# Performance work log

Measured on AMD Instinct MI355X. Metric: run time of the kernel, lower is better.

The kernel has to match this reference:

```python
import jax, jax.numpy as jnp
import numpy as np

OUT_H, OUT_W = 7, 7          # aligned_height, aligned_width
SPATIAL_SCALE = 0.25         # stride-4 feature level
SAMPLE_NUM = 2               # 2x2 bilinear samples per bin


def setup_inputs() -> dict:
    key = jax.random.key(0)
    kf, kb, kx, ky, kw, kh = jax.random.split(key, 6)
    B, C, H, W = 4, 256, 200, 272
    features = jax.random.normal(kf, (B, C, H, W), dtype=jnp.float32)
    N = 1024
    img_w = W / SPATIAL_SCALE  # boxes live in image coords
    img_h = H / SPATIAL_SCALE
    bi = jax.random.randint(kb, (N,), 0, B).astype(jnp.float32)
    x1 = jax.random.uniform(kx, (N,), dtype=jnp.float32) * (img_w - 260.0)
    y1 = jax.random.uniform(ky, (N,), dtype=jnp.float32) * (img_h - 260.0)
    bw = 16.0 + jax.random.uniform(kw, (N,), dtype=jnp.float32) * 240.0
    bh = 16.0 + jax.random.uniform(kh, (N,), dtype=jnp.float32) * 240.0
    rois = jnp.stack([bi, x1, y1, x1 + bw, y1 + bh], axis=1)  # [N,5]
    return {"features": features, "rois": rois}


def _roi_align(features, rois):
    B, C, H, W = features.shape
    N = rois.shape[0]
    sn = SAMPLE_NUM
    feats = jnp.transpose(features, (0, 2, 3, 1))  # [B,H,W,C] channel-last for gathers

    b = rois[:, 0].astype(jnp.int32)
    x1 = rois[:, 1] * SPATIAL_SCALE
    y1 = rois[:, 2] * SPATIAL_SCALE
    x2 = rois[:, 3] * SPATIAL_SCALE
    y2 = rois[:, 4] * SPATIAL_SCALE
    roi_w = jnp.maximum(x2 - x1, 1.0)
    roi_h = jnp.maximum(y2 - y1, 1.0)
    bin_w = roi_w / OUT_W
    bin_h = roi_h / OUT_H

    # flattened sample positions: y = y1 + (p + 0.5)/sn * bin_h,  p in [0, OUT_H*sn)
    py = (jnp.arange(OUT_H * sn, dtype=jnp.float32) + 0.5) / sn
    px = (jnp.arange(OUT_W * sn, dtype=jnp.float32) + 0.5) / sn
    ys = y1[:, None] + py[None, :] * bin_h[:, None]  # [N, Hs]
    xs = x1[:, None] + px[None, :] * bin_w[:, None]  # [N, Ws]

    valid = ((ys > -1.0) & (ys < H))[:, :, None] & ((xs > -1.0) & (xs < W))[:, None, :]

    y = jnp.clip(ys, 0.0, H - 1.0)
    x = jnp.clip(xs, 0.0, W - 1.0)
    y0 = jnp.clip(jnp.floor(y), 0.0, H - 2.0)
    x0 = jnp.clip(jnp.floor(x), 0.0, W - 2.0)
    ly = y - y0
    lx = x - x0
    hy = 1.0 - ly
    hx = 1.0 - lx
    y0i = y0.astype(jnp.int32)
    x0i = x0.astype(jnp.int32)
    y1i = y0i + 1
    x1i = x0i + 1

    bN = b[:, None, None]

    def g(yi, xi):  # gather corner values -> [N, Hs, Ws, C]
        return feats[bN, yi[:, :, None], xi[:, None, :]]

    w00 = (hy[:, :, None] * hx[:, None, :])[..., None]
    w01 = (hy[:, :, None] * lx[:, None, :])[..., None]
    w10 = (ly[:, :, None] * hx[:, None, :])[..., None]
    w11 = (ly[:, :, None] * lx[:, None, :])[..., None]

    val = (w00 * g(y0i, x0i) + w01 * g(y0i, x1i)
           + w10 * g(y1i, x0i) + w11 * g(y1i, x1i))
    val = jnp.where(valid[..., None], val, 0.0)

    # average the sn x sn samples per bin
    val = val.reshape(N, OUT_H, sn, OUT_W, sn, C).mean(axis=(2, 4))  # [N,OUT_H,OUT_W,C]
    return jnp.transpose(val, (0, 3, 1, 2))  # [N, C, OUT_H, OUT_W]


def reference(features, rois):
    return _roi_align(features, rois)
```

## Files before the change

### kernel.cpp

```cpp
#include <hip/hip_runtime.h>
#include <hip/hip_bf16.h>

#define B_ 4
#define C_ 256
#define H_ 200
#define W_ 272
#define OH 7
#define OW 7

__global__ void detect_dtype(const float* __restrict__ rois_f, int* __restrict__ flag) {
  if (threadIdx.x == 0 && blockIdx.x == 0) {
    bool ok = true;
    for (int k = 0; k < 8; ++k) {
      float v = rois_f[5 * k];
      ok = ok && (v >= 0.0f) && (v < 4.0f) && (v == floorf(v)) && (v == v);
    }
    *flag = ok ? 0 : 1;
  }
}

template <typename T> __device__ __forceinline__ float to_f(T v);
template <> __device__ __forceinline__ float to_f<float>(float v) { return v; }
template <> __device__ __forceinline__ float to_f<__hip_bfloat16>(__hip_bfloat16 v) {
  return __bfloat162float(v);
}
template <typename T> __device__ __forceinline__ T from_f(float v);
template <> __device__ __forceinline__ float from_f<float>(float v) { return v; }
template <> __device__ __forceinline__ __hip_bfloat16 from_f<__hip_bfloat16>(float v) {
  return __float2bfloat16(v);
}

template <typename T>
__device__ __forceinline__ void roi_align_body(const T* __restrict__ feats,
                                               const T* __restrict__ rois,
                                               T* __restrict__ out, int idx) {
  int pw = idx % OW;
  int ph = (idx / OW) % OH;
  int c  = (idx / (OW * OH)) % C_;
  int n  = idx / (OW * OH * C_);

  const T* r = rois + (size_t)n * 5;
  int   b  = (int)to_f<T>(r[0]);
  float x1 = to_f<T>(r[1]) * 0.25f;
  float y1 = to_f<T>(r[2]) * 0.25f;
  float x2 = to_f<T>(r[3]) * 0.25f;
  float y2 = to_f<T>(r[4]) * 0.25f;

  float bin_w = fmaxf(x2 - x1, 1.0f) * (1.0f / 7.0f);
  float bin_h = fmaxf(y2 - y1, 1.0f) * (1.0f / 7.0f);

  const T* fp = feats + ((size_t)b * C_ + c) * (size_t)(H_ * W_);

  float sum = 0.0f;
#pragma unroll
  for (int iy = 0; iy < 2; ++iy) {
    float ys = y1 + ((float)(ph * 2 + iy) + 0.5f) * 0.5f * bin_h;
    bool vy = (ys > -1.0f) && (ys < (float)H_);
    float y  = fminf(fmaxf(ys, 0.0f), (float)(H_ - 1));
    float y0f = fminf(floorf(y), (float)(H_ - 2));
    float ly = y - y0f;
    float hy = 1.0f - ly;
    int y0 = (int)y0f;

#pragma unroll
    for (int ix = 0; ix < 2; ++ix) {
      float xs = x1 + ((float)(pw * 2 + ix) + 0.5f) * 0.5f * bin_w;
      bool vx = (xs > -1.0f) && (xs < (float)W_);
      float x  = fminf(fmaxf(xs, 0.0f), (float)(W_ - 1));
      float x0f = fminf(floorf(x), (float)(W_ - 2));
      float lx = x - x0f;
      float hx = 1.0f - lx;
      int x0 = (int)x0f;

      const T* p = fp + y0 * W_ + x0;
      float v00 = to_f<T>(p[0]);
      float v01 = to_f<T>(p[1]);
      float v10 = to_f<T>(p[W_]);
      float v11 = to_f<T>(p[W_ + 1]);
      float v = hy * (hx * v00 + lx * v01) + ly * (hx * v10 + lx * v11);
      if (vy && vx) sum += v;
    }
  }

  out[idx] = from_f<T>(sum * 0.25f);
}

__global__ __launch_bounds__(256) void roi_align_kernel(
    const void* __restrict__ feats, const void* __restrict__ rois,
    void* __restrict__ out, const int* __restrict__ flag, int total) {
  int idx = blockIdx.x * blockDim.x + threadIdx.x;
  if (idx >= total) return;
  if (*flag == 0) {
    roi_align_body<float>((const float*)feats, (const float*)rois, (float*)out, idx);
  } else {
    roi_align_body<__hip_bfloat16>((const __hip_bfloat16*)feats,
                                   (const __hip_bfloat16*)rois,
                                   (__hip_bfloat16*)out, idx);
  }
}

extern "C" void kernel_launch(void* const* d_in, const int* in_sizes, int n_in,
                              void* d_out, int out_size, void* d_ws, size_t ws_size,
                              hipStream_t stream) {
  const void* feats = d_in[0];
  const void* rois  = d_in[1];
  int* flag = (int*)d_ws;

  detect_dtype<<<1, 64, 0, stream>>>((const float*)rois, flag);

  int total = out_size;
  int threads = 256;
  int blocks = (total + threads - 1) / threads;
  roi_align_kernel<<<blocks, threads, 0, stream>>>(feats, rois, d_out, flag, total);
}
```

Before: 460.2 us.

## Transpose features to NHWC in workspace and gather per-ROI across channels

Adds a tiled shared-memory NCHW-to-NHWC transpose into the workspace, then a per-ROI kernel where each thread handles one channel, so the bilinear corner loads are contiguous across a wavefront. Results are staged in shared memory and written back in the NCHW output order. It also removes the runtime dtype-detection launch and the bf16 path. This trades an extra full pass over the ~223MB feature tensor (read plus write) for coalesced gathers, and depends on the workspace being large enough, otherwise it falls back to the direct kernel.

```diff
diff --git a/kernel.cpp b/kernel.cpp
--- a/kernel.cpp
+++ b/kernel.cpp
@@ -1,56 +1,118 @@
 #include <hip/hip_runtime.h>
-#include <hip/hip_bf16.h>
 
 #define B_ 4
 #define C_ 256
 #define H_ 200
 #define W_ 272
+#define HW_ (H_ * W_)
 #define OH 7
 #define OW 7
+#define NROI 1024
 
-__global__ void detect_dtype(const float* __restrict__ rois_f, int* __restrict__ flag) {
-  if (threadIdx.x == 0 && blockIdx.x == 0) {
-    bool ok = true;
-    for (int k = 0; k < 8; ++k) {
-      float v = rois_f[5 * k];
-      ok = ok && (v >= 0.0f) && (v < 4.0f) && (v == floorf(v)) && (v == v);
-    }
-    *flag = ok ? 0 : 1;
+__global__ __launch_bounds__(256) void nchw_to_nhwc(
+    const float* __restrict__ in, float* __restrict__ out) {
+  __shared__ float tile[32][33];
+  int hw0 = blockIdx.x * 32;
+  int c0  = blockIdx.y * 32;
+  int b   = blockIdx.z;
+  int t = threadIdx.x;
+
+  int lhw = t & 31, lc = t >> 5;
+#pragma unroll
+  for (int i = 0; i < 4; ++i) {
+    int c = c0 + lc + i * 8;
+    tile[lc + i * 8][lhw] = in[((size_t)b * C_ + c) * HW_ + hw0 + lhw];
+  }
+  __syncthreads();
+  int wc = t & 31, whw = t >> 5;
+#pragma unroll
+  for (int i = 0; i < 4; ++i) {
+    int hw = hw0 + whw + i * 8;
+    out[((size_t)b * HW_ + hw) * C_ + c0 + wc] = tile[wc][whw + i * 8];
   }
 }
 
-template <typename T> __device__ __forceinline__ float to_f(T v);
-template <> __device__ __forceinline__ float to_f<float>(float v) { return v; }
-template <> __device__ __forceinline__ float to_f<__hip_bfloat16>(__hip_bfloat16 v) {
-  return __bfloat162float(v);
-}
-template <typename T> __device__ __forceinline__ T from_f(float v);
-template <> __device__ __forceinline__ float from_f<float>(float v) { return v; }
-template <> __device__ __forceinline__ __hip_bfloat16 from_f<__hip_bfloat16>(float v) {
-  return __float2bfloat16(v);
+__global__ __launch_bounds__(256) void roi_gather_nhwc(
+    const float* __restrict__ nhwc, const float* __restrict__ rois,
+    float* __restrict__ out) {
+  __shared__ float acc[C_ * 51];
+  int n = blockIdx.x;
+  int c = threadIdx.x;
+
+  const float* r = rois + (size_t)n * 5;
+  int   b  = (int)r[0];
+  float x1 = r[1] * 0.25f;
+  float y1 = r[2] * 0.25f;
+  float x2 = r[3] * 0.25f;
+  float y2 = r[4] * 0.25f;
+  float bin_w = fmaxf(x2 - x1, 1.0f) * (1.0f / 7.0f);
+  float bin_h = fmaxf(y2 - y1, 1.0f) * (1.0f / 7.0f);
+
+  const float* fb = nhwc + (size_t)b * HW_ * C_ + c;
+
+  for (int s = 0; s < 49; ++s) {
+    int ph = s / 7, pw = s % 7;
+    float sum = 0.0f;
+#pragma unroll
+    for (int iy = 0; iy < 2; ++iy) {
+      float ys = y1 + ((float)(ph * 2 + iy) + 0.5f) * 0.5f * bin_h;
+      bool vy = (ys > -1.0f) && (ys < (float)H_);
+      float y  = fminf(fmaxf(ys, 0.0f), (float)(H_ - 1));
+      float y0f = fminf(floorf(y), (float)(H_ - 2));
+      float ly = y - y0f;
+      float hy = 1.0f - ly;
+      int y0 = (int)y0f;
+#pragma unroll
+      for (int ix = 0; ix < 2; ++ix) {
+        float xs = x1 + ((float)(pw * 2 + ix) + 0.5f) * 0.5f * bin_w;
+        bool vx = (xs > -1.0f) && (xs < (float)W_);
+        float x  = fminf(fmaxf(xs, 0.0f), (float)(W_ - 1));
+        float x0f = fminf(floorf(x), (float)(W_ - 2));
+        float lx = x - x0f;
+        float hx = 1.0f - lx;
+        int x0 = (int)x0f;
+
+        const float* p = fb + (size_t)(y0 * W_ + x0) * C_;
+        float v00 = p[0];
+        float v01 = p[C_];
+        float v10 = p[W_ * C_];
+        float v11 = p[W_ * C_ + C_];
+        float v = hy * (hx * v00 + lx * v01) + ly * (hx * v10 + lx * v11);
+        if (vy && vx) sum += v;
+      }
+    }
+    acc[c * 51 + s] = sum * 0.25f;
+  }
+  __syncthreads();
+
+  float* o = out + (size_t)n * (C_ * 49);
+  for (int j = c; j < C_ * 49; j += 256) {
+    int cc = j / 49;
+    int ss = j - cc * 49;
+    o[j] = acc[cc * 51 + ss];
+  }
 }
 
-template <typename T>
-__device__ __forceinline__ void roi_align_body(const T* __restrict__ feats,
-                                               const T* __restrict__ rois,
-                                               T* __restrict__ out, int idx) {
+__global__ __launch_bounds__(256) void roi_align_direct(
+    const float* __restrict__ feats, const float* __restrict__ rois,
+    float* __restrict__ out, int total) {
+  int idx = blockIdx.x * blockDim.x + threadIdx.x;
+  if (idx >= total) return;
   int pw = idx % OW;
   int ph = (idx / OW) % OH;
   int c  = (idx / (OW * OH)) % C_;
   int n  = idx / (OW * OH * C_);
 
-  const T* r = rois + (size_t)n * 5;
-  int   b  = (int)to_f<T>(r[0]);
-  float x1 = to_f<T>(r[1]) * 0.25f;
-  float y1 = to_f<T>(r[2]) * 0.25f;
-  float x2 = to_f<T>(r[3]) * 0.25f;
-  float y2 = to_f<T>(r[4]) * 0.25f;
-
+  const float* r = rois + (size_t)n * 5;
+  int   b  = (int)r[0];
+  float x1 = r[1] * 0.25f;
+  float y1 = r[2] * 0.25f;
+  float x2 = r[3] * 0.25f;
+  float y2 = r[4] * 0.25f;
   float bin_w = fmaxf(x2 - x1, 1.0f) * (1.0f / 7.0f);
   float bin_h = fmaxf(y2 - y1, 1.0f) * (1.0f / 7.0f);
 
-  const T* fp = feats + ((size_t)b * C_ + c) * (size_t)(H_ * W_);
-
+  const float* fp = feats + ((size_t)b * C_ + c) * (size_t)HW_;
   float sum = 0.0f;
 #pragma unroll
   for (int iy = 0; iy < 2; ++iy) {
@@ -58,58 +120,40 @@
     bool vy = (ys > -1.0f) && (ys < (float)H_);
     float y  = fminf(fmaxf(ys, 0.0f), (float)(H_ - 1));
     float y0f = fminf(floorf(y), (float)(H_ - 2));
-    float ly = y - y0f;
-    float hy = 1.0f - ly;
+    float ly = y - y0f, hy = 1.0f - ly;
     int y0 = (int)y0f;
-
 #pragma unroll
     for (int ix = 0; ix < 2; ++ix) {
       float xs = x1 + ((float)(pw * 2 + ix) + 0.5f) * 0.5f * bin_w;
       bool vx = (xs > -1.0f) && (xs < (float)W_);
       float x  = fminf(fmaxf(xs, 0.0f), (float)(W_ - 1));
       float x0f = fminf(floorf(x), (float)(W_ - 2));
-      float lx = x - x0f;
-      float hx = 1.0f - lx;
+      float lx = x - x0f, hx = 1.0f - lx;
       int x0 = (int)x0f;
-
-      const T* p = fp + y0 * W_ + x0;
-      float v00 = to_f<T>(p[0]);
-      float v01 = to_f<T>(p[1]);
-      float v10 = to_f<T>(p[W_]);
-      float v11 = to_f<T>(p[W_ + 1]);
-      float v = hy * (hx * v00 + lx * v01) + ly * (hx * v10 + lx * v11);
+      const float* p = fp + y0 * W_ + x0;
+      float v = hy * (hx * p[0] + lx * p[1]) + ly * (hx * p[W_] + lx * p[W_ + 1]);
       if (vy && vx) sum += v;
     }
   }
-
-  out[idx] = from_f<T>(sum * 0.25f);
-}
-
-__global__ __launch_bounds__(256) void roi_align_kernel(
-    const void* __restrict__ feats, const void* __restrict__ rois,
-    void* __restrict__ out, const int* __restrict__ flag, int total) {
-  int idx = blockIdx.x * blockDim.x + threadIdx.x;
-  if (idx >= total) return;
-  if (*flag == 0) {
-    roi_align_body<float>((const float*)feats, (const float*)rois, (float*)out, idx);
-  } else {
-    roi_align_body<__hip_bfloat16>((const __hip_bfloat16*)feats,
-                                   (const __hip_bfloat16*)rois,
-                                   (__hip_bfloat16*)out, idx);
-  }
+  out[idx] = sum * 0.25f;
 }
 
 extern "C" void kernel_launch(void* const* d_in, const int* in_sizes, int n_in,
                               void* d_out, int out_size, void* d_ws, size_t ws_size,
                               hipStream_t stream) {
-  const void* feats = d_in[0];
-  const void* rois  = d_in[1];
-  int* flag = (int*)d_ws;
+  const float* feats = (const float*)d_in[0];
+  const float* rois  = (const float*)d_in[1];
+  float* out = (float*)d_out;
 
-  detect_dtype<<<1, 64, 0, stream>>>((const float*)rois, flag);
+  const size_t nhwc_bytes = (size_t)B_ * HW_ * C_ * sizeof(float);
 
-  int total = out_size;
-  int threads = 256;
-  int blocks = (total + threads - 1) / threads;
-  roi_align_kernel<<<blocks, threads, 0, stream>>>(feats, rois, d_out, flag, total);
+  if (ws_size >= nhwc_bytes) {
+    float* nhwc = (float*)d_ws;
+    dim3 tgrid(HW_ / 32, C_ / 32, B_);
+    nchw_to_nhwc<<<tgrid, 256, 0, stream>>>(feats, nhwc);
+    roi_gather_nhwc<<<NROI, 256, 0, stream>>>(nhwc, rois, out);
+  } else {
+    int total = out_size;
+    roi_align_direct<<<(total + 255) / 256, 256, 0, stream>>>(feats, rois, out, total);
+  }
 }
```

New measurement: 535.6 us. 1.16x slower.
